# Optimization experiments

Measured on AMD Instinct MI355X. Metric: run time of the kernel, lower is better.

## Reference

```python
import jax, jax.numpy as jnp
import numpy as np

NUM_LAYER = 5
HIDDEN = 128
PROJ = 256
ATOM_VOCAB = 128
BOND_VOCAB = 16
N_ATOM_FEATS = 9
N_BOND_FEATS = 3
BN_EPS = 1e-5


def _batchnorm(x, gamma, beta):
    # training-mode BatchNorm1d over the node axis
    mu = x.mean(axis=0)
    var = x.var(axis=0)
    return (x - mu) * jax.lax.rsqrt(var + BN_EPS) * gamma + beta


def setup_inputs() -> dict:
    key = jax.random.key(0)
    ks = jax.random.split(key, 16)
    N, E = 40000, 640000
    s = 0.05
    inp = {
        "x": jax.random.randint(ks[0], (N, N_ATOM_FEATS), 0, ATOM_VOCAB, dtype=jnp.int32),
        "edge_index": jax.random.randint(ks[1], (2, E), 0, N, dtype=jnp.int32),
        "edge_attr": jax.random.randint(ks[2], (E, N_BOND_FEATS), 0, BOND_VOCAB, dtype=jnp.int32),
        "atom_emb": jax.random.normal(ks[3], (N_ATOM_FEATS, ATOM_VOCAB, HIDDEN), jnp.float32) * s,
        "bond_emb": jax.random.normal(ks[4], (NUM_LAYER, N_BOND_FEATS, BOND_VOCAB, HIDDEN), jnp.float32) * s,
        "eps": jnp.zeros((NUM_LAYER,), jnp.float32),
        "w1": jax.random.normal(ks[5], (NUM_LAYER, HIDDEN, 2 * HIDDEN), jnp.float32) * s,
        "b1": jnp.zeros((NUM_LAYER, 2 * HIDDEN), jnp.float32),
        "bn1_g": jnp.ones((NUM_LAYER, 2 * HIDDEN), jnp.float32),
        "bn1_b": jnp.zeros((NUM_LAYER, 2 * HIDDEN), jnp.float32),
        "w2": jax.random.normal(ks[6], (NUM_LAYER, 2 * HIDDEN, HIDDEN), jnp.float32) * s,
        "b2": jnp.zeros((NUM_LAYER, HIDDEN), jnp.float32),
        "bn_g": jnp.ones((NUM_LAYER, HIDDEN), jnp.float32),
        "bn_b": jnp.zeros((NUM_LAYER, HIDDEN), jnp.float32),
        "lin_w": jax.random.normal(ks[7], (HIDDEN, PROJ), jnp.float32) * s,
        "lin_b": jnp.zeros((PROJ,), jnp.float32),
    }
    return inp


def reference(x, edge_index, edge_attr, atom_emb, bond_emb, eps, w1, b1, bn1_g, bn1_b, w2, b2, bn_g, bn_b, lin_w, lin_b):
    N = x.shape[0]
    src, dst = edge_index[0], edge_index[1]
    # AtomEncoder: sum of per-column embeddings -> [N, H]
    h = atom_emb[jnp.arange(N_ATOM_FEATS), x].sum(axis=1)
    for l in range(NUM_LAYER):
        # BondEncoder for this layer -> [E, H]
        e = bond_emb[l][jnp.arange(N_BOND_FEATS), edge_attr].sum(axis=1)
        # message: relu(x_j + edge_emb); aggregate: scatter-add to dst
        msg = jax.nn.relu(h[src] + e)
        agg = jax.ops.segment_sum(msg, dst, num_segments=N)
        z = (1.0 + eps[l]) * h + agg
        # GIN MLP: Linear -> BN -> ReLU -> Linear
        z = z @ w1[l] + b1[l]
        z = jax.nn.relu(_batchnorm(z, bn1_g[l], bn1_b[l]))
        z = z @ w2[l] + b2[l]
        # outer BatchNorm, relu except last layer
        h = _batchnorm(z, bn_g[l], bn_b[l])
        if l < NUM_LAYER - 1:
            h = jax.nn.relu(h)
    return h @ lin_w + lin_b
```

## Files before the change

### kernel.cpp

```cpp
#include <hip/hip_runtime.h>
#include <stdint.h>


typedef unsigned short ushort_t;
typedef unsigned int uint_t;
typedef __attribute__((ext_vector_type(8))) short bf16x8;
typedef __attribute__((ext_vector_type(16))) float f32x16;

#define MFMA32(a, b, c) __builtin_amdgcn_mfma_f32_32x32x16_bf16(a, b, c, 0, 0, 0)
#define NBANK 8
#define BANKSZ 768

__device__ inline ushort_t f2bf(float f) {
  uint_t u = __builtin_bit_cast(uint_t, f);
  u += 0x7FFFu + ((u >> 16) & 1u);
  return (ushort_t)(u >> 16);
}
__device__ inline float bf2f(uint_t h) {
  uint_t u = (h & 0xFFFFu) << 16;
  return __builtin_bit_cast(float, u);
}
__device__ inline uint_t pack2(float a, float b) {
  return (uint_t)f2bf(a) | ((uint_t)f2bf(b) << 16);
}
__device__ inline f32x16 zero16() {
  f32x16 z;
#pragma unroll
  for (int i = 0; i < 16; ++i) z[i] = 0.f;
  return z;
}


__global__ __launch_bounds__(256) void bond_comb_k(
    const float* __restrict__ bemb, ushort_t* __restrict__ comb)
{
  int idx = blockIdx.x * 256 + threadIdx.x;
  if (idx >= 5 * 4096 * 64) return;
  int lane = idx & 63, c = (idx >> 6) & 4095, l = idx >> 18;
  const float2* b2 = (const float2*)(bemb + (size_t)l * 3 * 16 * 128);
  float2 e0 = b2[(c & 15) * 64 + lane];
  float2 e1 = b2[(16 + ((c >> 4) & 15)) * 64 + lane];
  float2 e2 = b2[(32 + (c >> 8)) * 64 + lane];
  ((uint_t*)comb)[idx] = pack2(e0.x + e1.x + e2.x, e0.y + e1.y + e2.y);
}

__global__ __launch_bounds__(256) void swz_all_k(
    const float* __restrict__ w1, const float* __restrict__ linw,
    const float* __restrict__ w2, ushort_t* __restrict__ bswz1,
    ushort_t* __restrict__ bswz2)
{
  int t = blockIdx.x * 256 + threadIdx.x;
  if (t >= 11 * 4096) return;
  int m = t >> 12, tt = t & 4095, lane = tt & 63;
  if (m < 6) {
    const float* w = (m < 5) ? (w1 + (size_t)m * 32768) : linw;
    ushort_t* o = bswz1 + (size_t)m * 32768;
    int nt = (tt >> 6) & 7, s = tt >> 9;
    int kb = s * 16 + (lane >> 5) * 8, n = nt * 32 + (lane & 31);
    ushort_t tmp[8];
#pragma unroll
    for (int j = 0; j < 8; ++j) tmp[j] = f2bf(w[(size_t)(kb + j) * 256 + n]);
    ((uint4*)o)[tt] = *(uint4*)tmp;
  } else {
    int mm = m - 6;
    const float* w = w2 + (size_t)mm * 32768;
    ushort_t* o = bswz2 + (size_t)mm * 32768;
    int nt = (tt >> 6) & 3, s = tt >> 8;
    int kb = s * 16 + (lane >> 5) * 8, n = nt * 32 + (lane & 31);
    ushort_t tmp[8];
#pragma unroll
    for (int j = 0; j < 8; ++j) tmp[j] = f2bf(w[(size_t)(kb + j) * 128 + n]);
    ((uint4*)o)[tt] = *(uint4*)tmp;
  }
}


__global__ void zero_int_k(int* p, int n) {
  int i = blockIdx.x * 256 + threadIdx.x;
  if (i < n) p[i] = 0;
}

__global__ void hist_k(const int* __restrict__ ei, int* __restrict__ cnt, int E) {
  int e = blockIdx.x * 256 + threadIdx.x;
  if (e >= E) return;
  atomicAdd(&cnt[ei[E + e]], 1);
}

__global__ __launch_bounds__(256) void block_sum_k(
    const int* __restrict__ cnt, int* __restrict__ bsum, int N)
{
  __shared__ int red[256];
  int t = threadIdx.x, idx = blockIdx.x * 256 + t;
  red[t] = (idx < N) ? cnt[idx] : 0;
  __syncthreads();
  for (int o = 128; o > 0; o >>= 1) {
    if (t < o) red[t] += red[t + o];
    __syncthreads();
  }
  if (t == 0) bsum[blockIdx.x] = red[0];
}

__global__ __launch_bounds__(256) void scan_bsum_k(
    int* __restrict__ bsum, int* __restrict__ rsN, int nb)
{
  __shared__ int s[256];
  int t = threadIdx.x;
  s[t] = (t < nb) ? bsum[t] : 0;
  __syncthreads();
  for (int o = 1; o < 256; o <<= 1) {
    int v = (t >= o) ? s[t - o] : 0;
    __syncthreads();
    s[t] += v;
    __syncthreads();
  }
  if (t < nb) bsum[t] = (t == 0) ? 0 : s[t - 1];
  if (t == nb - 1) *rsN = s[t];
}

__global__ __launch_bounds__(256) void scan_write_k(
    const int* __restrict__ cnt, const int* __restrict__ bsum,
    int* __restrict__ rs, int* __restrict__ cursor, int N)
{
  __shared__ int s[256];
  int t = threadIdx.x, idx = blockIdx.x * 256 + t;
  int v = (idx < N) ? cnt[idx] : 0;
  s[t] = v;
  __syncthreads();
  for (int o = 1; o < 256; o <<= 1) {
    int u = (t >= o) ? s[t - o] : 0;
    __syncthreads();
    s[t] += u;
    __syncthreads();
  }
  int excl = s[t] - v + bsum[blockIdx.x];
  if (idx < N) { rs[idx] = excl; cursor[idx] = excl; }
}

__global__ void scatter_k(const int* __restrict__ ei, const int* __restrict__ ea,
                          int* __restrict__ cursor, uint32_t* __restrict__ sorted, int E)
{
  int e = blockIdx.x * 256 + threadIdx.x;
  if (e >= E) return;
  int src = ei[e], dst = ei[E + e];
  int a0 = ea[e * 3], a1 = ea[e * 3 + 1], a2 = ea[e * 3 + 2];
  int pos = atomicAdd(&cursor[dst], 1);
  sorted[pos] = (uint32_t)src | ((uint32_t)a0 << 16) | ((uint32_t)a1 << 20) | ((uint32_t)a2 << 24);
}


__global__ __launch_bounds__(256) void atom_encode_k(
    const int* __restrict__ x, const float* __restrict__ aemb,
    ushort_t* __restrict__ hbn, float* __restrict__ stats, int N)
{
  if (blockIdx.x == 0) {
    for (int i = threadIdx.x; i < NBANK * BANKSZ; i += 256) stats[i] = 0.f;
  }
  int idx = blockIdx.x * 256 + threadIdx.x;
  if (idx >= N * 64) return;
  int n = idx >> 6, lane = idx & 63;
  const int* xr = x + n * 9;
  float sx = 0.f, sy = 0.f;
#pragma unroll
  for (int f = 0; f < 9; ++f) {
    float2 e = ((const float2*)(aemb + (size_t)(f * 128 + xr[f]) * 128))[lane];
    sx += e.x; sy += e.y;
  }
  ((uint_t*)hbn)[idx] = pack2(sx, sy);
}

__global__ __launch_bounds__(256) void bnrelu_k(
    const float* __restrict__ raw, float* __restrict__ stats,
    const float* __restrict__ g, const float* __restrict__ bb,
    ushort_t* __restrict__ hbn, float invN, int total)
{
  if (blockIdx.x == 0) {
    for (int i = threadIdx.x; i < NBANK * 512; i += 256) {
      int b = i >> 9, c = i & 511;
      stats[b * BANKSZ + c] = 0.f;
    }
  }
  int t = blockIdx.x * 256 + threadIdx.x;
  int lane = t & 63;
  int c0 = 2 * lane, c1 = c0 + 1;
  float s0 = 0.f, q0 = 0.f, s1 = 0.f, q1 = 0.f;
#pragma unroll
  for (int b = 0; b < NBANK; ++b) {
    const float* bk = stats + b * BANKSZ + 512;
    s0 += bk[c0]; q0 += bk[128 + c0];
    s1 += bk[c1]; q1 += bk[128 + c1];
  }
  float mu0 = s0 * invN, mu1 = s1 * invN;
  float v0 = q0 * invN - mu0 * mu0;
  float v1 = q1 * invN - mu1 * mu1;
  float scx = rsqrtf(v0 + 1e-5f) * g[c0];
  float scy = rsqrtf(v1 + 1e-5f) * g[c1];
  float shx = bb[c0] - mu0 * scx;
  float shy = bb[c1] - mu1 * scy;
  int stride = gridDim.x * 256;
  for (int idx = t; idx < total; idx += stride) {
    float2 h = ((const float2*)raw)[idx];
    float hx = fmaxf(fmaf(h.x, scx, shx), 0.f);
    float hy = fmaxf(fmaf(h.y, scy, shy), 0.f);
    ((uint_t*)hbn)[idx] = pack2(hx, hy);
  }
}

__global__ __launch_bounds__(256) void aggregate_k(
    const ushort_t* __restrict__ hbn, const ushort_t* __restrict__ comb,
    const uint32_t* __restrict__ sorted, const int* __restrict__ rs,
    const float* __restrict__ eps, int layer, uint2* zinout, int N)
{
  int wave = threadIdx.x >> 6, lane = threadIdx.x & 63;
  int n = blockIdx.x * 4 + wave;
  if (n >= N) return;
  int beg = rs[n], end = rs[n + 1];
  const uint_t* hb = (const uint_t*)hbn;
  const uint_t* cb = ((const uint_t*)comb) + (size_t)layer * 4096 * 64;
  float ax = 0.f, ay = 0.f;
  int i = beg;
  for (; i + 16 <= end; i += 16) {
    uint32_t p[16];
#pragma unroll
    for (int j = 0; j < 16; ++j) p[j] = sorted[i + j];
    uint_t hv[16], ee[16];
#pragma unroll
    for (int j = 0; j < 16; ++j) {
      hv[j] = hb[(size_t)(p[j] & 0xFFFFu) * 64 + lane];
      ee[j] = cb[(p[j] >> 16) * 64 + lane];
    }
#pragma unroll
    for (int j = 0; j < 16; ++j) {
      ax += fmaxf(bf2f(hv[j]) + bf2f(ee[j]), 0.f);
      ay += fmaxf(bf2f(hv[j] >> 16) + bf2f(ee[j] >> 16), 0.f);
    }
  }
  for (; i + 4 <= end; i += 4) {
    uint32_t p[4];
#pragma unroll
    for (int j = 0; j < 4; ++j) p[j] = sorted[i + j];
    uint_t hv[4], ee[4];
#pragma unroll
    for (int j = 0; j < 4; ++j) {
      hv[j] = hb[(size_t)(p[j] & 0xFFFFu) * 64 + lane];
      ee[j] = cb[(p[j] >> 16) * 64 + lane];
    }
#pragma unroll
    for (int j = 0; j < 4; ++j) {
      ax += fmaxf(bf2f(hv[j]) + bf2f(ee[j]), 0.f);
      ay += fmaxf(bf2f(hv[j] >> 16) + bf2f(ee[j] >> 16), 0.f);
    }
  }
  for (; i < end; ++i) {
    uint32_t p = sorted[i];
    uint_t ee = cb[(p >> 16) * 64 + lane];
    uint_t hv = hb[(size_t)(p & 0xFFFFu) * 64 + lane];
    ax += fmaxf(bf2f(hv) + bf2f(ee), 0.f);
    ay += fmaxf(bf2f(hv >> 16) + bf2f(ee >> 16), 0.f);
  }
  float s = 1.f + eps[layer];
  uint_t hn = hb[(size_t)n * 64 + lane];
  float zx = fmaf(s, bf2f(hn), ax);
  float zy = fmaf(s, bf2f(hn >> 16), ay);
  ushort_t hxz = f2bf(zx), hyz = f2bf(zy);
  float lox = zx - bf2f(hxz), loy = zy - bf2f(hyz);
  uint2 o;
  o.x = (uint_t)hxz | ((uint_t)hyz << 16);
  o.y = pack2(lox, loy);
  zinout[(size_t)n * 64 + lane] = o;
}

__global__ __launch_bounds__(512, 4) void gemm1_k(
    const uint2* zin, const ushort_t* __restrict__ bswz,
    const float* __restrict__ bias, ushort_t* z1bf,
    float* __restrict__ stats)
{
  __shared__ ushort_t As[64 * 128];
  __shared__ ushort_t Al[64 * 128];
  int tid = threadIdx.x;
  int wave = tid >> 6, lane = tid & 63;
  int row0 = blockIdx.x * 64;
  if (blockIdx.x == 0) {
    for (int i = tid; i < NBANK * 256; i += 512) {
      int b = i >> 8, c = i & 255;
      stats[b * BANKSZ + 512 + c] = 0.f;
    }
  }
  {
    const uint2* src = zin + (size_t)row0 * 64;
#pragma unroll
    for (int i = 0; i < 8; ++i) {
      int idx = tid + 512 * i;
      int r = idx >> 6, l = idx & 63, c = 2 * l;
      uint2 v = src[idx];
      int scol = (((c >> 3) ^ (r & 15)) << 3) | (c & 7);
      *(uint_t*)&As[r * 128 + scol] = v.x;
      *(uint_t*)&Al[r * 128 + scol] = v.y;
    }
  }
  __syncthreads();
  int lr = lane & 31, half = lane >> 5;
  int nt = wave;
  f32x16 acc0 = zero16(), acc1 = zero16();
  const bf16x8* Bp = (const bf16x8*)bswz;
#pragma unroll
  for (int s = 0; s < 8; ++s) {
    int k = s * 16 + half * 8;
    int scol = ((k >> 3) ^ (lr & 15)) << 3;
    bf16x8 b = Bp[(s * 8 + nt) * 64 + lane];
    bf16x8 ah0 = *(const bf16x8*)&As[lr * 128 + scol];
    bf16x8 al0 = *(const bf16x8*)&Al[lr * 128 + scol];
    bf16x8 ah1 = *(const bf16x8*)&As[(32 + lr) * 128 + scol];
    bf16x8 al1 = *(const bf16x8*)&Al[(32 + lr) * 128 + scol];
    acc0 = MFMA32(ah0, b, acc0);
    acc0 = MFMA32(al0, b, acc0);
    acc1 = MFMA32(ah1, b, acc1);
    acc1 = MFMA32(al1, b, acc1);
  }
  int col = nt * 32 + lr;
  float bv = bias[col];
  float s0 = 0.f, q0 = 0.f;
#pragma unroll
  for (int r2 = 0; r2 < 16; ++r2) {
    int rrow = (r2 & 3) + 8 * (r2 >> 2) + 4 * half;
    float v0 = acc0[r2] + bv;
    float v1 = acc1[r2] + bv;
    z1bf[(size_t)(row0 + rrow) * 256 + col] = f2bf(v0);
    z1bf[(size_t)(row0 + 32 + rrow) * 256 + col] = f2bf(v1);
    s0 += v0 + v1;
    q0 += v0 * v0 + v1 * v1;
  }
  s0 += __shfl_xor(s0, 32);
  q0 += __shfl_xor(q0, 32);
  if (lane < 32) {
    float* bk = stats + (blockIdx.x & (NBANK - 1)) * BANKSZ;
    atomicAdd(&bk[col], s0);
    atomicAdd(&bk[256 + col], q0);
  }
}

__global__ __launch_bounds__(256) void mlp2_k(
    float* rawz, float* __restrict__ stats,
    const float* __restrict__ g1, const float* __restrict__ bb1,
    const ushort_t* __restrict__ bswz2, const float* __restrict__ b2,
    float invN)
{
  __shared__ ushort_t Bs[64 * 256];
  __shared__ float sc1[256], sh1[256];
  int tid = threadIdx.x;
  int wave = tid >> 6, lane = tid & 63;
  int lr = lane & 31, half = lane >> 5;
  int row0 = blockIdx.x * 64;
  {
    float s = 0.f, q = 0.f;
#pragma unroll
    for (int b = 0; b < NBANK; ++b) {
      const float* bk = stats + b * BANKSZ;
      s += bk[tid];
      q += bk[256 + tid];
    }
    float mu = s * invN;
    float var = q * invN - mu * mu;
    float r = rsqrtf(var + 1e-5f) * g1[tid];
    sc1[tid] = r;
    sh1[tid] = bb1[tid] - mu * r;
  }
  __syncthreads();
  {
    const uint4* src = (const uint4*)((const ushort_t*)rawz + (size_t)row0 * 256);
#pragma unroll
    for (int i = 0; i < 8; ++i) {
      int idx = tid + 256 * i;
      int r = idx >> 5, c = (idx & 31) * 8;
      uint4 v = src[idx];
      float f0 = fmaxf(fmaf(bf2f(v.x), sc1[c], sh1[c]), 0.f);
      float f1 = fmaxf(fmaf(bf2f(v.x >> 16), sc1[c + 1], sh1[c + 1]), 0.f);
      float f2 = fmaxf(fmaf(bf2f(v.y), sc1[c + 2], sh1[c + 2]), 0.f);
      float f3 = fmaxf(fmaf(bf2f(v.y >> 16), sc1[c + 3], sh1[c + 3]), 0.f);
      float f4 = fmaxf(fmaf(bf2f(v.z), sc1[c + 4], sh1[c + 4]), 0.f);
      float f5 = fmaxf(fmaf(bf2f(v.z >> 16), sc1[c + 5], sh1[c + 5]), 0.f);
      float f6 = fmaxf(fmaf(bf2f(v.w), sc1[c + 6], sh1[c + 6]), 0.f);
      float f7 = fmaxf(fmaf(bf2f(v.w >> 16), sc1[c + 7], sh1[c + 7]), 0.f);
      uint4 o;
      o.x = pack2(f0, f1);
      o.y = pack2(f2, f3);
      o.z = pack2(f4, f5);
      o.w = pack2(f6, f7);
      int scol = ((c >> 3) ^ (r & 15)) << 3;
      *(uint4*)&Bs[r * 256 + scol] = o;
    }
  }
  __syncthreads();
  f32x16 acc0 = zero16(), acc1 = zero16();
  {
    const bf16x8* Bp2 = (const bf16x8*)bswz2;
#pragma unroll
    for (int s = 0; s < 16; ++s) {
      int k = s * 16 + half * 8;
      int scol = ((k >> 3) ^ (lr & 15)) << 3;
      bf16x8 a0 = *(const bf16x8*)&Bs[lr * 256 + scol];
      bf16x8 a1 = *(const bf16x8*)&Bs[(32 + lr) * 256 + scol];
      bf16x8 b = Bp2[(s * 4 + wave) * 64 + lane];
      acc0 = MFMA32(a0, b, acc0);
      acc1 = MFMA32(a1, b, acc1);
    }
  }
  int col = wave * 32 + lr;
  float bv = b2[col];
  float s0 = 0.f, q0 = 0.f;
  auto emit = [&](const f32x16& a, int mtb) {
#pragma unroll
    for (int r2 = 0; r2 < 16; ++r2) {
      int row = row0 + mtb + (r2 & 3) + 8 * (r2 >> 2) + 4 * half;
      float v = a[r2] + bv;
      rawz[(size_t)row * 128 + col] = v;
      s0 += v;
      q0 += v * v;
    }
  };
  emit(acc0, 0);
  emit(acc1, 32);
  s0 += __shfl_xor(s0, 32);
  q0 += __shfl_xor(q0, 32);
  if (lane < 32) {
    float* bk = stats + (blockIdx.x & (NBANK - 1)) * BANKSZ + 512;
    atomicAdd(&bk[col], s0);
    atomicAdd(&bk[128 + col], q0);
  }
}

__global__ __launch_bounds__(256) void final_proj_k(
    const float* __restrict__ inf, const ushort_t* __restrict__ bswz,
    const float* __restrict__ bias, const float* __restrict__ stats,
    const float* __restrict__ g, const float* __restrict__ bb,
    float* __restrict__ outf, float invN)
{
  __shared__ ushort_t As[64 * 128];
  __shared__ float sc[128], sh[128];
  int tid = threadIdx.x;
  int wave = tid >> 6, lane = tid & 63;
  int lr = lane & 31, half = lane >> 5;
  int row0 = blockIdx.x * 64;
  if (tid < 128) {
    int c = tid;
    float s = 0.f, q = 0.f;
#pragma unroll
    for (int b = 0; b < NBANK; ++b) {
      const float* bk = stats + b * BANKSZ + 512;
      s += bk[c];
      q += bk[128 + c];
    }
    float mu = s * invN;
    float var = q * invN - mu * mu;
    float r = rsqrtf(var + 1e-5f) * g[c];
    sc[c] = r;
    sh[c] = bb[c] - mu * r;
  }
  __syncthreads();
  {
    const float4* src = (const float4*)(inf + (size_t)row0 * 128);
#pragma unroll
    for (int i = 0; i < 8; ++i) {
      int idx = tid + 256 * i;
      int r = idx >> 5, c = (idx & 31) * 4;
      float4 v = src[idx];
      v.x = fmaf(v.x, sc[c], sh[c]);
      v.y = fmaf(v.y, sc[c + 1], sh[c + 1]);
      v.z = fmaf(v.z, sc[c + 2], sh[c + 2]);
      v.w = fmaf(v.w, sc[c + 3], sh[c + 3]);
      uint2 o;
      o.x = pack2(v.x, v.y);
      o.y = pack2(v.z, v.w);
      int scol = (((c >> 3) ^ (r & 15)) << 3) | (c & 7);
      *(uint2*)&As[r * 128 + scol] = o;
    }
  }
  __syncthreads();
  int nt0 = wave * 2, nt1 = nt0 + 1;
  f32x16 acc00 = zero16(), acc01 = zero16(), acc10 = zero16(), acc11 = zero16();
  const bf16x8* Bp = (const bf16x8*)bswz;
#pragma unroll
  for (int s = 0; s < 8; ++s) {
    int k = s * 16 + half * 8;
    int scol = ((k >> 3) ^ (lr & 15)) << 3;
    bf16x8 a0 = *(const bf16x8*)&As[lr * 128 + scol];
    bf16x8 a1 = *(const bf16x8*)&As[(32 + lr) * 128 + scol];
    bf16x8 b0 = Bp[(s * 8 + nt0) * 64 + lane];
    bf16x8 b1 = Bp[(s * 8 + nt1) * 64 + lane];
    acc00 = MFMA32(a0, b0, acc00);
    acc10 = MFMA32(a1, b0, acc10);
    acc01 = MFMA32(a0, b1, acc01);
    acc11 = MFMA32(a1, b1, acc11);
  }
  int col0 = nt0 * 32 + lr, col1 = nt1 * 32 + lr;
  float bv0 = bias[col0], bv1 = bias[col1];
  auto emit = [&](const f32x16& a, int mtb, int col, float bv) {
#pragma unroll
    for (int r2 = 0; r2 < 16; ++r2) {
      int row = row0 + mtb + (r2 & 3) + 8 * (r2 >> 2) + 4 * half;
      outf[(size_t)row * 256 + col] = a[r2] + bv;
    }
  };
  emit(acc00, 0, col0, bv0);
  emit(acc10, 32, col0, bv0);
  emit(acc01, 0, col1, bv1);
  emit(acc11, 32, col1, bv1);
}

extern "C" void kernel_launch(void* const* d_in, const int* in_sizes, int n_in,
                              void* d_out, int out_size, void* d_ws, size_t ws_size,
                              hipStream_t stream)
{
  const int* x = (const int*)d_in[0];
  const int* ei = (const int*)d_in[1];
  const int* ea = (const int*)d_in[2];
  const float* aemb = (const float*)d_in[3];
  const float* bemb = (const float*)d_in[4];
  const float* eps = (const float*)d_in[5];
  const float* w1 = (const float*)d_in[6];
  const float* b1 = (const float*)d_in[7];
  const float* bn1g = (const float*)d_in[8];
  const float* bn1b = (const float*)d_in[9];
  const float* w2 = (const float*)d_in[10];
  const float* b2 = (const float*)d_in[11];
  const float* bng = (const float*)d_in[12];
  const float* bnb = (const float*)d_in[13];
  const float* linw = (const float*)d_in[14];
  const float* linb = (const float*)d_in[15];
  int N = in_sizes[0] / 9;
  int E = in_sizes[1] / 2;
  int nb = (N + 255) / 256;

  char* ws = (char*)d_ws;
  size_t off = 0;
  auto alloc = [&](size_t bytes) {
    void* p = ws + off;
    off += (bytes + 255) & ~(size_t)255;
    return p;
  };
  float* raw = (float*)alloc((size_t)N * 128 * 4);
  ushort_t* hbn = (ushort_t*)alloc((size_t)N * 128 * 2);
  ushort_t* comb = (ushort_t*)alloc((size_t)5 * 4096 * 128 * 2);
  ushort_t* bswz1 = (ushort_t*)alloc((size_t)6 * 32768 * 2);
  ushort_t* bswz2 = (ushort_t*)alloc((size_t)5 * 32768 * 2);
  uint32_t* sorted = (uint32_t*)alloc((size_t)E * 4);
  int* rs = (int*)alloc((size_t)(N + 1) * 4);
  int* cursor = (int*)alloc((size_t)N * 4);
  int* cnt = (int*)alloc((size_t)N * 4);
  int* bsum = (int*)alloc((size_t)nb * 4);
  float* stats = (float*)alloc((size_t)NBANK * BANKSZ * 4);
  float invN = 1.f / (float)N;

  bond_comb_k<<<(5 * 4096 * 64 + 255) / 256, 256, 0, stream>>>(bemb, comb);
  swz_all_k<<<(11 * 4096 + 255) / 256, 256, 0, stream>>>(w1, linw, w2, bswz1, bswz2);

  atom_encode_k<<<(N * 64 + 255) / 256, 256, 0, stream>>>(x, aemb, hbn, stats, N);
  zero_int_k<<<(N + 255) / 256, 256, 0, stream>>>(cnt, N);
  hist_k<<<(E + 255) / 256, 256, 0, stream>>>(ei, cnt, E);
  block_sum_k<<<nb, 256, 0, stream>>>(cnt, bsum, N);
  scan_bsum_k<<<1, 256, 0, stream>>>(bsum, rs + N, nb);
  scan_write_k<<<nb, 256, 0, stream>>>(cnt, bsum, rs, cursor, N);
  scatter_k<<<(E + 255) / 256, 256, 0, stream>>>(ei, ea, cursor, sorted, E);

  for (int l = 0; l < 5; ++l) {
    if (l > 0) {
      bnrelu_k<<<2048, 256, 0, stream>>>(
          raw, stats, bng + (size_t)(l - 1) * 128,
          bnb + (size_t)(l - 1) * 128, hbn, invN, N * 64);
    }
    aggregate_k<<<(N + 3) / 4, 256, 0, stream>>>(
        hbn, comb, sorted, rs, eps, l, (uint2*)raw, N);
    gemm1_k<<<N / 64, 512, 0, stream>>>(
        (const uint2*)raw, bswz1 + (size_t)l * 32768, b1 + (size_t)l * 256,
        (ushort_t*)raw, stats);
    mlp2_k<<<N / 64, 256, 0, stream>>>(
        raw, stats, bn1g + (size_t)l * 256, bn1b + (size_t)l * 256,
        bswz2 + (size_t)l * 32768, b2 + (size_t)l * 128,
        invN);
  }
  final_proj_k<<<N / 64, 256, 0, stream>>>(
      raw, bswz1 + (size_t)5 * 32768, linb, stats,
      bng + (size_t)4 * 128, bnb + (size_t)4 * 128, (float*)d_out, invN);
}
```

Baseline: 529.3 us.

## Fuse neighbor aggregation with first MLP GEMM using 16x16 MFMA tiles

```diff
diff --git a/kernel.cpp b/kernel.cpp
--- a/kernel.cpp
+++ b/kernel.cpp
@@ -5,10 +5,12 @@
 typedef unsigned short ushort_t;
 typedef unsigned int uint_t;
 typedef __attribute__((ext_vector_type(8))) short bf16x8;
+typedef __attribute__((ext_vector_type(4))) float f32x4;
 typedef __attribute__((ext_vector_type(16))) float f32x16;
 
 #define MFMA32(a, b, c) __builtin_amdgcn_mfma_f32_32x32x16_bf16(a, b, c, 0, 0, 0)
-#define NBANK 8
+#define MFMA16(a, b, c) __builtin_amdgcn_mfma_f32_16x16x32_bf16(a, b, c, 0, 0, 0)
+#define NBANK 32
 #define BANKSZ 768
 
 __device__ inline ushort_t f2bf(float f) {
@@ -47,10 +49,10 @@
 __global__ __launch_bounds__(256) void swz_all_k(
     const float* __restrict__ w1, const float* __restrict__ linw,
     const float* __restrict__ w2, ushort_t* __restrict__ bswz1,
-    ushort_t* __restrict__ bswz2)
+    ushort_t* __restrict__ bswz2, ushort_t* __restrict__ bswz16)
 {
   int t = blockIdx.x * 256 + threadIdx.x;
-  if (t >= 11 * 4096) return;
+  if (t >= 16 * 4096) return;
   int m = t >> 12, tt = t & 4095, lane = tt & 63;
   if (m < 6) {
     const float* w = (m < 5) ? (w1 + (size_t)m * 32768) : linw;
@@ -61,7 +63,7 @@
 #pragma unroll
     for (int j = 0; j < 8; ++j) tmp[j] = f2bf(w[(size_t)(kb + j) * 256 + n]);
     ((uint4*)o)[tt] = *(uint4*)tmp;
-  } else {
+  } else if (m < 11) {
     int mm = m - 6;
     const float* w = w2 + (size_t)mm * 32768;
     ushort_t* o = bswz2 + (size_t)mm * 32768;
@@ -70,6 +72,16 @@
     ushort_t tmp[8];
 #pragma unroll
     for (int j = 0; j < 8; ++j) tmp[j] = f2bf(w[(size_t)(kb + j) * 128 + n]);
+    ((uint4*)o)[tt] = *(uint4*)tmp;
+  } else {
+    int mm = m - 11;
+    const float* w = w1 + (size_t)mm * 32768;
+    ushort_t* o = bswz16 + (size_t)mm * 32768;
+    int nt = (tt >> 6) & 15, kk = tt >> 10;
+    int kb = kk * 32 + (lane >> 4) * 8, n = nt * 16 + (lane & 15);
+    ushort_t tmp[8];
+#pragma unroll
+    for (int j = 0; j < 8; ++j) tmp[j] = f2bf(w[(size_t)(kb + j) * 256 + n]);
     ((uint4*)o)[tt] = *(uint4*)tmp;
   }
 }
@@ -205,133 +217,108 @@
   }
 }
 
-__global__ __launch_bounds__(256) void aggregate_k(
+__global__ __launch_bounds__(1024, 8) void agg_gemm1_k(
     const ushort_t* __restrict__ hbn, const ushort_t* __restrict__ comb,
     const uint32_t* __restrict__ sorted, const int* __restrict__ rs,
-    const float* __restrict__ eps, int layer, uint2* zinout, int N)
-{
-  int wave = threadIdx.x >> 6, lane = threadIdx.x & 63;
-  int n = blockIdx.x * 4 + wave;
-  if (n >= N) return;
-  int beg = rs[n], end = rs[n + 1];
-  const uint_t* hb = (const uint_t*)hbn;
-  const uint_t* cb = ((const uint_t*)comb) + (size_t)layer * 4096 * 64;
-  float ax = 0.f, ay = 0.f;
-  int i = beg;
-  for (; i + 16 <= end; i += 16) {
-    uint32_t p[16];
-#pragma unroll
-    for (int j = 0; j < 16; ++j) p[j] = sorted[i + j];
-    uint_t hv[16], ee[16];
-#pragma unroll
-    for (int j = 0; j < 16; ++j) {
-      hv[j] = hb[(size_t)(p[j] & 0xFFFFu) * 64 + lane];
-      ee[j] = cb[(p[j] >> 16) * 64 + lane];
-    }
-#pragma unroll
-    for (int j = 0; j < 16; ++j) {
-      ax += fmaxf(bf2f(hv[j]) + bf2f(ee[j]), 0.f);
-      ay += fmaxf(bf2f(hv[j] >> 16) + bf2f(ee[j] >> 16), 0.f);
-    }
-  }
-  for (; i + 4 <= end; i += 4) {
-    uint32_t p[4];
-#pragma unroll
-    for (int j = 0; j < 4; ++j) p[j] = sorted[i + j];
-    uint_t hv[4], ee[4];
-#pragma unroll
-    for (int j = 0; j < 4; ++j) {
-      hv[j] = hb[(size_t)(p[j] & 0xFFFFu) * 64 + lane];
-      ee[j] = cb[(p[j] >> 16) * 64 + lane];
-    }
-#pragma unroll
-    for (int j = 0; j < 4; ++j) {
-      ax += fmaxf(bf2f(hv[j]) + bf2f(ee[j]), 0.f);
-      ay += fmaxf(bf2f(hv[j] >> 16) + bf2f(ee[j] >> 16), 0.f);
-    }
-  }
-  for (; i < end; ++i) {
-    uint32_t p = sorted[i];
-    uint_t ee = cb[(p >> 16) * 64 + lane];
-    uint_t hv = hb[(size_t)(p & 0xFFFFu) * 64 + lane];
-    ax += fmaxf(bf2f(hv) + bf2f(ee), 0.f);
-    ay += fmaxf(bf2f(hv >> 16) + bf2f(ee >> 16), 0.f);
-  }
-  float s = 1.f + eps[layer];
-  uint_t hn = hb[(size_t)n * 64 + lane];
-  float zx = fmaf(s, bf2f(hn), ax);
-  float zy = fmaf(s, bf2f(hn >> 16), ay);
-  ushort_t hxz = f2bf(zx), hyz = f2bf(zy);
-  float lox = zx - bf2f(hxz), loy = zy - bf2f(hyz);
-  uint2 o;
-  o.x = (uint_t)hxz | ((uint_t)hyz << 16);
-  o.y = pack2(lox, loy);
-  zinout[(size_t)n * 64 + lane] = o;
-}
-
-__global__ __launch_bounds__(512, 4) void gemm1_k(
-    const uint2* zin, const ushort_t* __restrict__ bswz,
-    const float* __restrict__ bias, ushort_t* z1bf,
-    float* __restrict__ stats)
-{
-  __shared__ ushort_t As[64 * 128];
-  __shared__ ushort_t Al[64 * 128];
+    const float* __restrict__ eps, int layer,
+    const ushort_t* __restrict__ bswz16, const float* __restrict__ bias,
+    ushort_t* __restrict__ z1bf, float* __restrict__ stats, int N)
+{
+  __shared__ ushort_t As[16 * 128];
+  __shared__ ushort_t Al[16 * 128];
   int tid = threadIdx.x;
   int wave = tid >> 6, lane = tid & 63;
-  int row0 = blockIdx.x * 64;
+  int row0 = blockIdx.x * 16;
   if (blockIdx.x == 0) {
-    for (int i = tid; i < NBANK * 256; i += 512) {
-      int b = i >> 8, c = i & 255;
-      stats[b * BANKSZ + 512 + c] = 0.f;
+    for (int i = tid; i < NBANK * 256; i += 1024) {
+      stats[(i >> 8) * BANKSZ + 512 + (i & 255)] = 0.f;
     }
   }
   {
-    const uint2* src = zin + (size_t)row0 * 64;
-#pragma unroll
-    for (int i = 0; i < 8; ++i) {
-      int idx = tid + 512 * i;
-      int r = idx >> 6, l = idx & 63, c = 2 * l;
-      uint2 v = src[idx];
-      int scol = (((c >> 3) ^ (r & 15)) << 3) | (c & 7);
-      *(uint_t*)&As[r * 128 + scol] = v.x;
-      *(uint_t*)&Al[r * 128 + scol] = v.y;
-    }
-  }
-  __syncthreads();
-  int lr = lane & 31, half = lane >> 5;
-  int nt = wave;
-  f32x16 acc0 = zero16(), acc1 = zero16();
-  const bf16x8* Bp = (const bf16x8*)bswz;
-#pragma unroll
-  for (int s = 0; s < 8; ++s) {
-    int k = s * 16 + half * 8;
-    int scol = ((k >> 3) ^ (lr & 15)) << 3;
-    bf16x8 b = Bp[(s * 8 + nt) * 64 + lane];
-    bf16x8 ah0 = *(const bf16x8*)&As[lr * 128 + scol];
-    bf16x8 al0 = *(const bf16x8*)&Al[lr * 128 + scol];
-    bf16x8 ah1 = *(const bf16x8*)&As[(32 + lr) * 128 + scol];
-    bf16x8 al1 = *(const bf16x8*)&Al[(32 + lr) * 128 + scol];
-    acc0 = MFMA32(ah0, b, acc0);
-    acc0 = MFMA32(al0, b, acc0);
-    acc1 = MFMA32(ah1, b, acc1);
-    acc1 = MFMA32(al1, b, acc1);
-  }
-  int col = nt * 32 + lr;
+    int n = row0 + wave;
+    int beg = rs[n], end = rs[n + 1];
+    const uint_t* hb = (const uint_t*)hbn;
+    const uint_t* cb = ((const uint_t*)comb) + (size_t)layer * 4096 * 64;
+    float ax = 0.f, ay = 0.f;
+    int i = beg;
+    for (; i + 16 <= end; i += 16) {
+      uint32_t p[16];
+#pragma unroll
+      for (int j = 0; j < 16; ++j) p[j] = sorted[i + j];
+      uint_t hv[16], ee[16];
+#pragma unroll
+      for (int j = 0; j < 16; ++j) {
+        hv[j] = hb[(size_t)(p[j] & 0xFFFFu) * 64 + lane];
+        ee[j] = cb[(p[j] >> 16) * 64 + lane];
+      }
+#pragma unroll
+      for (int j = 0; j < 16; ++j) {
+        ax += fmaxf(bf2f(hv[j]) + bf2f(ee[j]), 0.f);
+        ay += fmaxf(bf2f(hv[j] >> 16) + bf2f(ee[j] >> 16), 0.f);
+      }
+    }
+    for (; i + 4 <= end; i += 4) {
+      uint32_t p[4];
+#pragma unroll
+      for (int j = 0; j < 4; ++j) p[j] = sorted[i + j];
+      uint_t hv[4], ee[4];
+#pragma unroll
+      for (int j = 0; j < 4; ++j) {
+        hv[j] = hb[(size_t)(p[j] & 0xFFFFu) * 64 + lane];
+        ee[j] = cb[(p[j] >> 16) * 64 + lane];
+      }
+#pragma unroll
+      for (int j = 0; j < 4; ++j) {
+        ax += fmaxf(bf2f(hv[j]) + bf2f(ee[j]), 0.f);
+        ay += fmaxf(bf2f(hv[j] >> 16) + bf2f(ee[j] >> 16), 0.f);
+      }
+    }
+    for (; i < end; ++i) {
+      uint32_t p = sorted[i];
+      uint_t ee = cb[(p >> 16) * 64 + lane];
+      uint_t hv = hb[(size_t)(p & 0xFFFFu) * 64 + lane];
+      ax += fmaxf(bf2f(hv) + bf2f(ee), 0.f);
+      ay += fmaxf(bf2f(hv >> 16) + bf2f(ee >> 16), 0.f);
+    }
+    float s = 1.f + eps[layer];
+    uint_t hn = ((const uint_t*)hbn)[(size_t)n * 64 + lane];
+    float zx = fmaf(s, bf2f(hn), ax);
+    float zy = fmaf(s, bf2f(hn >> 16), ay);
+    ushort_t hxz = f2bf(zx), hyz = f2bf(zy);
+    float lox = zx - bf2f(hxz), loy = zy - bf2f(hyz);
+    int c = 2 * lane;
+    int scol = (((c >> 3) ^ (wave & 15)) << 3) | (c & 7);
+    *(uint_t*)&As[wave * 128 + scol] = (uint_t)hxz | ((uint_t)hyz << 16);
+    *(uint_t*)&Al[wave * 128 + scol] = pack2(lox, loy);
+  }
+  __syncthreads();
+  int m16 = lane & 15, kq = lane >> 4;
+  f32x4 acc = {0.f, 0.f, 0.f, 0.f};
+  const bf16x8* Bp = (const bf16x8*)bswz16;
+#pragma unroll
+  for (int kk = 0; kk < 4; ++kk) {
+    int cc = kk * 32 + kq * 8;
+    int sc = ((cc >> 3) ^ m16) << 3;
+    bf16x8 ah = *(const bf16x8*)&As[m16 * 128 + sc];
+    bf16x8 al = *(const bf16x8*)&Al[m16 * 128 + sc];
+    bf16x8 b = Bp[(kk * 16 + wave) * 64 + lane];
+    acc = MFMA16(ah, b, acc);
+    acc = MFMA16(al, b, acc);
+  }
+  int col = wave * 16 + m16;
   float bv = bias[col];
   float s0 = 0.f, q0 = 0.f;
 #pragma unroll
-  for (int r2 = 0; r2 < 16; ++r2) {
-    int rrow = (r2 & 3) + 8 * (r2 >> 2) + 4 * half;
-    float v0 = acc0[r2] + bv;
-    float v1 = acc1[r2] + bv;
-    z1bf[(size_t)(row0 + rrow) * 256 + col] = f2bf(v0);
-    z1bf[(size_t)(row0 + 32 + rrow) * 256 + col] = f2bf(v1);
-    s0 += v0 + v1;
-    q0 += v0 * v0 + v1 * v1;
-  }
-  s0 += __shfl_xor(s0, 32);
-  q0 += __shfl_xor(q0, 32);
-  if (lane < 32) {
+  for (int r = 0; r < 4; ++r) {
+    int rowl = kq * 4 + r;
+    float v = acc[r] + bv;
+    z1bf[(size_t)(row0 + rowl) * 256 + col] = f2bf(v);
+    s0 += v;
+    q0 += v * v;
+  }
+  s0 += __shfl_xor(s0, 16); q0 += __shfl_xor(q0, 16);
+  s0 += __shfl_xor(s0, 32); q0 += __shfl_xor(q0, 32);
+  if (lane < 16) {
     float* bk = stats + (blockIdx.x & (NBANK - 1)) * BANKSZ;
     atomicAdd(&bk[col], s0);
     atomicAdd(&bk[256 + col], q0);
@@ -542,6 +529,7 @@
   ushort_t* comb = (ushort_t*)alloc((size_t)5 * 4096 * 128 * 2);
   ushort_t* bswz1 = (ushort_t*)alloc((size_t)6 * 32768 * 2);
   ushort_t* bswz2 = (ushort_t*)alloc((size_t)5 * 32768 * 2);
+  ushort_t* bswz16 = (ushort_t*)alloc((size_t)5 * 32768 * 2);
   uint32_t* sorted = (uint32_t*)alloc((size_t)E * 4);
   int* rs = (int*)alloc((size_t)(N + 1) * 4);
   int* cursor = (int*)alloc((size_t)N * 4);
@@ -551,7 +539,8 @@
   float invN = 1.f / (float)N;
 
   bond_comb_k<<<(5 * 4096 * 64 + 255) / 256, 256, 0, stream>>>(bemb, comb);
-  swz_all_k<<<(11 * 4096 + 255) / 256, 256, 0, stream>>>(w1, linw, w2, bswz1, bswz2);
+  swz_all_k<<<(16 * 4096 + 255) / 256, 256, 0, stream>>>(
+      w1, linw, w2, bswz1, bswz2, bswz16);
 
   atom_encode_k<<<(N * 64 + 255) / 256, 256, 0, stream>>>(x, aemb, hbn, stats, N);
   zero_int_k<<<(N + 255) / 256, 256, 0, stream>>>(cnt, N);
@@ -567,11 +556,10 @@
           raw, stats, bng + (size_t)(l - 1) * 128,
           bnb + (size_t)(l - 1) * 128, hbn, invN, N * 64);
     }
-    aggregate_k<<<(N + 3) / 4, 256, 0, stream>>>(
-        hbn, comb, sorted, rs, eps, l, (uint2*)raw, N);
-    gemm1_k<<<N / 64, 512, 0, stream>>>(
-        (const uint2*)raw, bswz1 + (size_t)l * 32768, b1 + (size_t)l * 256,
-        (ushort_t*)raw, stats);
+    agg_gemm1_k<<<N / 16, 1024, 0, stream>>>(
+        hbn, comb, sorted, rs, eps, l,
+        bswz16 + (size_t)l * 32768, b1 + (size_t)l * 256,
+        (ushort_t*)raw, stats, N);
     mlp2_k<<<N / 64, 256, 0, stream>>>(
         raw, stats, bn1g + (size_t)l * 256, bn1b + (size_t)l * 256,
         bswz2 + (size_t)l * 32768, b2 + (size_t)l * 128,
```

Measured after the change: 578.0 us. 9.2% more time.
